# Performance work log

Hardware: AMD Instinct MI355X
Metric: run time of the kernel (lower is better)

## Reference

```python
import jax, jax.numpy as jnp
import numpy as np

E, D, H, T = 16, 1024, 4096, 8192  # num_expert, d_model, d_hidden (4h), total tokens


def setup_inputs() -> dict:
    key = jax.random.key(0)
    k0, k1, k2, k3, k4 = jax.random.split(key, 5)
    inp = jax.random.normal(k0, (T, D), dtype=jnp.float32)
    # FMoELinear init: kaiming-uniform-like, bound = 1/sqrt(fan_in)
    s1 = 1.0 / np.sqrt(D)
    s2 = 1.0 / np.sqrt(H)
    w1 = jax.random.uniform(k1, (E, H, D), jnp.float32, -s1, s1)  # htoh4 weight [E, out, in]
    b1 = jax.random.uniform(k2, (E, H), jnp.float32, -s1, s1)
    w2 = jax.random.uniform(k3, (E, D, H), jnp.float32, -s2, s2)  # h4toh weight
    b2 = jax.random.uniform(k4, (E, D), jnp.float32, -s2, s2)
    fwd_expert_count = jnp.full((E,), T // E, dtype=jnp.int32)  # tokens per expert (sums to T)
    return dict(inp=inp, w1=w1, b1=b1, w2=w2, b2=b2, fwd_expert_count=fwd_expert_count)


def reference(inp, w1, b1, w2, b2, fwd_expert_count):
    # Grouped GEMM: tokens are sorted by expert; segment e gets expert e's FFN.
    counts = np.asarray(fwd_expert_count)          # static per-expert row counts
    offs = np.concatenate([[0], np.cumsum(counts)])
    outs = []
    for e in range(counts.shape[0]):               # loop over fixed small expert set
        seg = inp[offs[e]:offs[e + 1]]             # [n_e, D]
        h = seg @ w1[e].T + b1[e]                  # htoh4: [n_e, H]
        h = jax.nn.gelu(h, approximate=False)      # torch F.gelu default (exact)
        outs.append(h @ w2[e].T + b2[e])           # h4toh: [n_e, D]
    return jnp.concatenate(outs, axis=0)           # [T, D]
```

## Files before the change

kernel.cpp:

```cpp
#include <hip/hip_runtime.h>
#include <hip/hip_bf16.h>

typedef float f32x4 __attribute__((ext_vector_type(4)));
typedef __bf16 bf16x8 __attribute__((ext_vector_type(8)));
typedef unsigned short u16;
typedef unsigned short u16x4 __attribute__((ext_vector_type(4)));
typedef unsigned short u16x8 __attribute__((ext_vector_type(8)));

#define BM 128
#define BN 128
#define BK 32
#define NT 256

__device__ __forceinline__ u16 f2bf(float f) {
  __bf16 h = (__bf16)f;
  return __builtin_bit_cast(u16, h);
}

template<bool A_BF16, bool DO_GELU, bool OUT_BF16>
__global__ __launch_bounds__(NT)
void ffn_gemm(const void* __restrict__ Ain, const float* __restrict__ Bw,
              const float* __restrict__ bias, void* __restrict__ Out,
              const int* __restrict__ counts, int E, int T, int N, int K)
{
  int mt = blockIdx.y;
  int row0 = 0, cnt = 0, e = 0;
  for (; e < E; ++e) {
    cnt = counts[e];
    int ntl = (cnt + BM - 1) / BM;
    if (mt < ntl) break;
    mt -= ntl; row0 += cnt;
  }
  if (e >= E) return;
  int valid = cnt - mt * BM; if (valid > BM) valid = BM;
  row0 += mt * BM;
  const int n0 = blockIdx.x * BN;

  const float* Be = Bw + (long long)e * N * K;
  const float* be = bias + (long long)e * N;

  __shared__ u16 As[2][BM][BK];
  __shared__ u16 Bs[2][BN][BK];

  const int t = threadIdx.x;
  const int lane = t & 63;
  const int w = t >> 6, wr = w >> 1, wc = w & 1;

  f32x4 acc[4][4];
#pragma unroll
  for (int i = 0; i < 4; ++i)
#pragma unroll
    for (int j = 0; j < 4; ++j) acc[i][j] = (f32x4){0.f, 0.f, 0.f, 0.f};

  const int NKT = K / BK;

  long long offA[4];
  if constexpr (!A_BF16) {
#pragma unroll
    for (int i = 0; i < 4; ++i) {
      int c = i * NT + t;
      int row = c >> 3, col = (c & 7) << 2;
      int gr = row0 + row; if (gr > T - 1) gr = T - 1;
      offA[i] = (long long)gr * K + col;
    }
  } else {
#pragma unroll
    for (int i = 0; i < 2; ++i) {
      int c = i * NT + t;
      int row = c >> 2, col = (c & 3) << 3;
      int gr = row0 + row; if (gr > T - 1) gr = T - 1;
      offA[i] = (long long)gr * K + col;
    }
  }
  long long offB[4];
#pragma unroll
  for (int i = 0; i < 4; ++i) {
    int c = i * NT + t;
    int row = c >> 3, col = (c & 7) << 2;
    offB[i] = (long long)(n0 + row) * K + col;
  }

  float rA[16]; u16x8 rAu[2]; float rB[16];

  auto load_g = [&](int kt) {
    const int k0 = kt * BK;
    if constexpr (!A_BF16) {
      const float* Af = (const float*)Ain;
#pragma unroll
      for (int i = 0; i < 4; ++i) {
        f32x4 v = *(const f32x4*)(Af + offA[i] + k0);
        rA[i*4+0] = v[0]; rA[i*4+1] = v[1]; rA[i*4+2] = v[2]; rA[i*4+3] = v[3];
      }
    } else {
      const u16* Ab = (const u16*)Ain;
#pragma unroll
      for (int i = 0; i < 2; ++i)
        rAu[i] = *(const u16x8*)(Ab + offA[i] + k0);
    }
#pragma unroll
    for (int i = 0; i < 4; ++i) {
      f32x4 v = *(const f32x4*)(Be + offB[i] + k0);
      rB[i*4+0] = v[0]; rB[i*4+1] = v[1]; rB[i*4+2] = v[2]; rB[i*4+3] = v[3];
    }
  };

  auto store_tile = [&](int buf) {
    if constexpr (!A_BF16) {
#pragma unroll
      for (int i = 0; i < 4; ++i) {
        int c = i * NT + t;
        int row = c >> 3, col = (c & 7) << 2;
        int kg = (col >> 3) ^ ((row >> 1) & 3);
        int off = kg * 8 + ((col >> 2) & 1) * 4;
        u16x4 pk = { f2bf(rA[i*4+0]), f2bf(rA[i*4+1]), f2bf(rA[i*4+2]), f2bf(rA[i*4+3]) };
        *(u16x4*)&As[buf][row][off] = pk;
      }
    } else {
#pragma unroll
      for (int i = 0; i < 2; ++i) {
        int c = i * NT + t;
        int row = c >> 2, col = (c & 3) << 3;
        int kg = (col >> 3) ^ ((row >> 1) & 3);
        *(u16x8*)&As[buf][row][kg * 8] = rAu[i];
      }
    }
#pragma unroll
    for (int i = 0; i < 4; ++i) {
      int c = i * NT + t;
      int row = c >> 3, col = (c & 7) << 2;
      int kg = (col >> 3) ^ ((row >> 1) & 3);
      int off = kg * 8 + ((col >> 2) & 1) * 4;
      u16x4 pk = { f2bf(rB[i*4+0]), f2bf(rB[i*4+1]), f2bf(rB[i*4+2]), f2bf(rB[i*4+3]) };
      *(u16x4*)&Bs[buf][row][off] = pk;
    }
  };

  load_g(0);
  store_tile(0);
  load_g(1);
  __syncthreads();

  for (int kt = 0; kt < NKT; ++kt) {
    const int cur = kt & 1;

    bf16x8 af[4], bfr[4];
    const int rl = lane & 15;
    const int kg = (lane >> 4) ^ ((rl >> 1) & 3);
#pragma unroll
    for (int mf = 0; mf < 4; ++mf)
      af[mf] = __builtin_bit_cast(bf16x8, *(const u16x8*)&As[cur][wr*64 + mf*16 + rl][kg*8]);
#pragma unroll
    for (int nf = 0; nf < 4; ++nf)
      bfr[nf] = __builtin_bit_cast(bf16x8, *(const u16x8*)&Bs[cur][wc*64 + nf*16 + rl][kg*8]);

    if (kt + 1 < NKT) store_tile(cur ^ 1);
    if (kt + 2 < NKT) load_g(kt + 2);

#pragma unroll
    for (int mf = 0; mf < 4; ++mf)
#pragma unroll
      for (int nf = 0; nf < 4; ++nf)
        acc[mf][nf] = __builtin_amdgcn_mfma_f32_16x16x32_bf16(af[mf], bfr[nf], acc[mf][nf], 0, 0, 0);

    if (kt + 1 < NKT) __syncthreads();
  }

  const int cl = lane & 15, rg = lane >> 4;
#pragma unroll
  for (int mf = 0; mf < 4; ++mf) {
#pragma unroll
    for (int nf = 0; nf < 4; ++nf) {
      int gcol = n0 + wc*64 + nf*16 + cl;
      float bv = be[gcol];
#pragma unroll
      for (int r = 0; r < 4; ++r) {
        int lrow = wr*64 + mf*16 + rg*4 + r;
        if (lrow < valid) {
          float v = acc[mf][nf][r] + bv;
          if constexpr (DO_GELU)
            v = 0.5f * v * (1.0f + erff(v * 0.70710678118654752f));
          long long idx = (long long)(row0 + lrow) * N + gcol;
          if constexpr (OUT_BF16) ((u16*)Out)[idx] = f2bf(v);
          else                    ((float*)Out)[idx] = v;
        }
      }
    }
  }
}

extern "C" void kernel_launch(void* const* d_in, const int* in_sizes, int n_in,
                              void* d_out, int out_size, void* d_ws, size_t ws_size,
                              hipStream_t stream) {
  const float* inp = (const float*)d_in[0];
  const float* w1  = (const float*)d_in[1];
  const float* b1  = (const float*)d_in[2];
  const float* w2  = (const float*)d_in[3];
  const float* b2  = (const float*)d_in[4];
  const int* cnts  = (const int*)d_in[5];

  const int E = in_sizes[5];
  const int H = in_sizes[2] / E;
  const int D = in_sizes[4] / E;
  const int T = in_sizes[0] / D;

  u16* hbuf = (u16*)d_ws;

  const int tiles = (T + BM - 1) / BM + E;
  dim3 blk(NT);

  dim3 g1(H / BN, tiles);
  ffn_gemm<false, true, true><<<g1, blk, 0, stream>>>(
      (const void*)inp, w1, b1, (void*)hbuf, cnts, E, T, H, D);

  dim3 g2(D / BN, tiles);
  ffn_gemm<true, false, false><<<g2, blk, 0, stream>>>(
      (const void*)hbuf, w2, b2, d_out, cnts, E, T, D, H);
}
```

Before: 328.8 us.

## Add dedicated 256x256-tile kernel for first FFN GEMM with 8 waves

Adds a specialized kernel for the first GEMM (input times w1, with GELU) that uses 256x256 output tiles, 512 threads and 8x4 MFMA fragments per wave. Each wave now reads from LDS a larger share of the operands it computes with, and the fp32 global traffic per FLOP drops, since the fp32 loads and bf16 conversion happen in the mainloop. It also precomputes swizzled LDS offsets and raises wave priority around the MFMA block. The cost is a much larger accumulator register footprint (128 floats per thread), which may lower occupancy. There are also fewer blocks (16 column tiles by 48 row tiles), which could underfill the GPU.

```diff
diff --git a/kernel.cpp b/kernel.cpp
--- a/kernel.cpp
+++ b/kernel.cpp
@@ -7,15 +7,156 @@
 typedef unsigned short u16x4 __attribute__((ext_vector_type(4)));
 typedef unsigned short u16x8 __attribute__((ext_vector_type(8)));
 
+__device__ __forceinline__ u16 f2bf(float f) {
+  __bf16 h = (__bf16)f;
+  return __builtin_bit_cast(u16, h);
+}
+
+#define G1_BM 256
+#define G1_BN 256
+#define G1_BK 32
+#define G1_NT 512
+
+__global__ __launch_bounds__(G1_NT, 2)
+void ffn_gemm1(const float* __restrict__ Af, const float* __restrict__ Bw,
+               const float* __restrict__ bias, u16* __restrict__ Out,
+               const int* __restrict__ counts, int E, int T, int N, int K)
+{
+  int mt = blockIdx.y;
+  int row0 = 0, cnt = 0, e = 0;
+  for (; e < E; ++e) {
+    cnt = counts[e];
+    int ntl = (cnt + G1_BM - 1) / G1_BM;
+    if (mt < ntl) break;
+    mt -= ntl; row0 += cnt;
+  }
+  if (e >= E) return;
+  int valid = cnt - mt * G1_BM; if (valid > G1_BM) valid = G1_BM;
+  row0 += mt * G1_BM;
+  const int n0 = blockIdx.x * G1_BN;
+  const float* Be = Bw + (long long)e * N * K;
+  const float* be = bias + (long long)e * N;
+
+  __shared__ u16 As[2][G1_BM * G1_BK];
+  __shared__ u16 Bs[2][G1_BN * G1_BK];
+
+  const int t = threadIdx.x;
+  const int lane = t & 63;
+  const int w = t >> 6, wr = w >> 2, wc = w & 3;
+
+  f32x4 acc[8][4];
+#pragma unroll
+  for (int i = 0; i < 8; ++i)
+#pragma unroll
+    for (int j = 0; j < 4; ++j) acc[i][j] = (f32x4){0.f, 0.f, 0.f, 0.f};
+
+  const int NKT = K / G1_BK;
+
+  long long offA[4]; int wAo[4];
+  long long offB[4]; int wBo[4];
+#pragma unroll
+  for (int i = 0; i < 4; ++i) {
+    int idx = i * G1_NT + t;
+    int row = idx >> 3, col4 = idx & 7;
+    int gr = row0 + row; if (gr > T - 1) gr = T - 1;
+    offA[i] = (long long)gr * K + col4 * 4;
+    wAo[i] = row * G1_BK + (((col4 >> 1) ^ (row & 3)) << 3) + ((col4 & 1) << 2);
+    offB[i] = (long long)(n0 + row) * K + col4 * 4;
+    wBo[i] = wAo[i] - ((row0 + row <= T - 1 ? 0 : 0));
+    wBo[i] = row * G1_BK + (((col4 >> 1) ^ (row & 3)) << 3) + ((col4 & 1) << 2);
+  }
+
+  const int rl = lane & 15, kgr = lane >> 4;
+  int aoff[8], boff[4];
+#pragma unroll
+  for (int mf = 0; mf < 8; ++mf) {
+    int row = wr * 128 + mf * 16 + rl;
+    aoff[mf] = row * G1_BK + ((kgr ^ (rl & 3)) << 3);
+  }
+#pragma unroll
+  for (int nf = 0; nf < 4; ++nf) {
+    int row = wc * 64 + nf * 16 + rl;
+    boff[nf] = row * G1_BK + ((kgr ^ (rl & 3)) << 3);
+  }
+
+  f32x4 a4[4], b4[4];
+
+  auto load_g = [&](int kt) {
+    const int k0 = kt * G1_BK;
+#pragma unroll
+    for (int i = 0; i < 4; ++i) a4[i] = *(const f32x4*)(Af + offA[i] + k0);
+#pragma unroll
+    for (int i = 0; i < 4; ++i) b4[i] = *(const f32x4*)(Be + offB[i] + k0);
+  };
+
+  auto store_tile = [&](int buf) {
+#pragma unroll
+    for (int i = 0; i < 4; ++i) {
+      u16x4 pa = { f2bf(a4[i][0]), f2bf(a4[i][1]), f2bf(a4[i][2]), f2bf(a4[i][3]) };
+      *(u16x4*)&As[buf][wAo[i]] = pa;
+    }
+#pragma unroll
+    for (int i = 0; i < 4; ++i) {
+      u16x4 pb = { f2bf(b4[i][0]), f2bf(b4[i][1]), f2bf(b4[i][2]), f2bf(b4[i][3]) };
+      *(u16x4*)&Bs[buf][wBo[i]] = pb;
+    }
+  };
+
+  load_g(0);
+  store_tile(0);
+  load_g(1);
+  __syncthreads();
+
+#pragma unroll 2
+  for (int kt = 0; kt < NKT; ++kt) {
+    const int cur = kt & 1;
+
+    bf16x8 bfr[4], af[8];
+#pragma unroll
+    for (int nf = 0; nf < 4; ++nf)
+      bfr[nf] = __builtin_bit_cast(bf16x8, *(const u16x8*)&Bs[cur][boff[nf]]);
+#pragma unroll
+    for (int mf = 0; mf < 8; ++mf)
+      af[mf] = __builtin_bit_cast(bf16x8, *(const u16x8*)&As[cur][aoff[mf]]);
+
+    if (kt + 1 < NKT) store_tile(cur ^ 1);
+    if (kt + 2 < NKT) load_g(kt + 2);
+
+    __builtin_amdgcn_s_setprio(1);
+#pragma unroll
+    for (int mf = 0; mf < 8; ++mf)
+#pragma unroll
+      for (int nf = 0; nf < 4; ++nf)
+        acc[mf][nf] = __builtin_amdgcn_mfma_f32_16x16x32_bf16(af[mf], bfr[nf], acc[mf][nf], 0, 0, 0);
+    __builtin_amdgcn_s_setprio(0);
+
+    __syncthreads();
+  }
+
+  const int cl = lane & 15, rg = lane >> 4;
+#pragma unroll
+  for (int nf = 0; nf < 4; ++nf) {
+    int gcol = n0 + wc * 64 + nf * 16 + cl;
+    float bv = be[gcol];
+#pragma unroll
+    for (int mf = 0; mf < 8; ++mf) {
+#pragma unroll
+      for (int r = 0; r < 4; ++r) {
+        int lrow = wr * 128 + mf * 16 + rg * 4 + r;
+        if (lrow < valid) {
+          float v = acc[mf][nf][r] + bv;
+          v = 0.5f * v * (1.0f + erff(v * 0.70710678118654752f));
+          Out[(long long)(row0 + lrow) * N + gcol] = f2bf(v);
+        }
+      }
+    }
+  }
+}
+
 #define BM 128
 #define BN 128
 #define BK 32
 #define NT 256
-
-__device__ __forceinline__ u16 f2bf(float f) {
-  __bf16 h = (__bf16)f;
-  return __builtin_bit_cast(u16, h);
-}
 
 template<bool A_BF16, bool DO_GELU, bool OUT_BF16>
 __global__ __launch_bounds__(NT)
@@ -205,14 +346,12 @@
 
   u16* hbuf = (u16*)d_ws;
 
-  const int tiles = (T + BM - 1) / BM + E;
-  dim3 blk(NT);
-
-  dim3 g1(H / BN, tiles);
-  ffn_gemm<false, true, true><<<g1, blk, 0, stream>>>(
-      (const void*)inp, w1, b1, (void*)hbuf, cnts, E, T, H, D);
-
-  dim3 g2(D / BN, tiles);
-  ffn_gemm<true, false, false><<<g2, blk, 0, stream>>>(
+  const int tiles1 = (T + G1_BM - 1) / G1_BM + E;
+  dim3 g1(H / G1_BN, tiles1);
+  ffn_gemm1<<<g1, dim3(G1_NT), 0, stream>>>(inp, w1, b1, hbuf, cnts, E, T, H, D);
+
+  const int tiles2 = (T + BM - 1) / BM + E;
+  dim3 g2(D / BN, tiles2);
+  ffn_gemm<true, false, false><<<g2, dim3(NT), 0, stream>>>(
       (const void*)hbuf, w2, b2, d_out, cnts, E, T, D, H);
 }
```

Result: faster. 315.3 us (-4.1%).

## Pre-convert input to bf16 and loop multiple N tiles per block in GEMM1

Applied to the files above, without the earlier changes.

Adds a separate kernel that converts the fp32 input activations to bf16 once, so the first GEMM reads bf16 A tiles instead of converting fp32 in every block. The first GEMM now has each block process four consecutive N tiles, shrinking the grid and reusing the block's expert lookup. The expert lookup loads the counts into a register array with vector loads. Costs are an extra launch and more workspace, and a smaller grid for GEMM1 that may reduce occupancy, with the same B weight traffic.

```diff
diff --git a/kernel.cpp b/kernel.cpp
--- a/kernel.cpp
+++ b/kernel.cpp
@@ -2,6 +2,7 @@
 #include <hip/hip_bf16.h>
 
 typedef float f32x4 __attribute__((ext_vector_type(4)));
+typedef int   i32x4 __attribute__((ext_vector_type(4)));
 typedef __bf16 bf16x8 __attribute__((ext_vector_type(8)));
 typedef unsigned short u16;
 typedef unsigned short u16x4 __attribute__((ext_vector_type(4)));
@@ -11,30 +12,53 @@
 #define BN 128
 #define BK 32
 #define NT 256
+#define MAXE 32
 
 __device__ __forceinline__ u16 f2bf(float f) {
   __bf16 h = (__bf16)f;
   return __builtin_bit_cast(u16, h);
 }
 
-template<bool A_BF16, bool DO_GELU, bool OUT_BF16>
+__global__ __launch_bounds__(256)
+void cvt_bf16(const float* __restrict__ in, u16* __restrict__ out, int n8) {
+  int i = blockIdx.x * 256 + threadIdx.x;
+  if (i < n8) {
+    f32x4 a = *(const f32x4*)(in + (long long)i * 8);
+    f32x4 b = *(const f32x4*)(in + (long long)i * 8 + 4);
+    u16x8 r = { f2bf(a[0]), f2bf(a[1]), f2bf(a[2]), f2bf(a[3]),
+                f2bf(b[0]), f2bf(b[1]), f2bf(b[2]), f2bf(b[3]) };
+    *(u16x8*)(out + (long long)i * 8) = r;
+  }
+}
+
+template<bool DO_GELU, bool OUT_BF16, int NTB>
 __global__ __launch_bounds__(NT)
-void ffn_gemm(const void* __restrict__ Ain, const float* __restrict__ Bw,
+void ffn_gemm(const u16* __restrict__ Ain, const float* __restrict__ Bw,
               const float* __restrict__ bias, void* __restrict__ Out,
               const int* __restrict__ counts, int E, int T, int N, int K)
 {
-  int mt = blockIdx.y;
-  int row0 = 0, cnt = 0, e = 0;
-  for (; e < E; ++e) {
-    cnt = counts[e];
-    int ntl = (cnt + BM - 1) / BM;
-    if (mt < ntl) break;
-    mt -= ntl; row0 += cnt;
-  }
-  if (e >= E) return;
+  int cs[MAXE];
+#pragma unroll
+  for (int j = 0; j < MAXE / 4; ++j) {
+    if (j * 4 + 3 < E) {
+      *(i32x4*)&cs[j * 4] = *(const i32x4*)(counts + j * 4);
+    } else {
+#pragma unroll
+      for (int q = 0; q < 4; ++q) cs[j*4+q] = (j*4+q < E) ? counts[j*4+q] : 0;
+    }
+  }
+  int mt = blockIdx.y, row0 = 0, e = -1, cnt = 0;
+#pragma unroll
+  for (int i = 0; i < MAXE; ++i) {
+    if (i < E && e < 0) {
+      int ntl = (cs[i] + BM - 1) / BM;
+      if (mt < ntl) { e = i; cnt = cs[i]; }
+      else { mt -= ntl; row0 += cs[i]; }
+    }
+  }
+  if (e < 0) return;
   int valid = cnt - mt * BM; if (valid > BM) valid = BM;
   row0 += mt * BM;
-  const int n0 = blockIdx.x * BN;
 
   const float* Be = Bw + (long long)e * N * K;
   const float* be = bias + (long long)e * N;
@@ -45,143 +69,121 @@
   const int t = threadIdx.x;
   const int lane = t & 63;
   const int w = t >> 6, wr = w >> 1, wc = w & 1;
-
-  f32x4 acc[4][4];
-#pragma unroll
-  for (int i = 0; i < 4; ++i)
-#pragma unroll
-    for (int j = 0; j < 4; ++j) acc[i][j] = (f32x4){0.f, 0.f, 0.f, 0.f};
-
   const int NKT = K / BK;
 
-  long long offA[4];
-  if constexpr (!A_BF16) {
-#pragma unroll
-    for (int i = 0; i < 4; ++i) {
-      int c = i * NT + t;
-      int row = c >> 3, col = (c & 7) << 2;
-      int gr = row0 + row; if (gr > T - 1) gr = T - 1;
-      offA[i] = (long long)gr * K + col;
-    }
-  } else {
-#pragma unroll
-    for (int i = 0; i < 2; ++i) {
-      int c = i * NT + t;
-      int row = c >> 2, col = (c & 3) << 3;
-      int gr = row0 + row; if (gr > T - 1) gr = T - 1;
-      offA[i] = (long long)gr * K + col;
-    }
-  }
-  long long offB[4];
+  long long offA[2];
+#pragma unroll
+  for (int i = 0; i < 2; ++i) {
+    int c = i * NT + t;
+    int row = c >> 2, col = (c & 3) << 3;
+    int gr = row0 + row; if (gr > T - 1) gr = T - 1;
+    offA[i] = (long long)gr * K + col;
+  }
+  int rBrow[4], rBcol[4];
 #pragma unroll
   for (int i = 0; i < 4; ++i) {
     int c = i * NT + t;
-    int row = c >> 3, col = (c & 7) << 2;
-    offB[i] = (long long)(n0 + row) * K + col;
-  }
-
-  float rA[16]; u16x8 rAu[2]; float rB[16];
-
-  auto load_g = [&](int kt) {
-    const int k0 = kt * BK;
-    if constexpr (!A_BF16) {
-      const float* Af = (const float*)Ain;
+    rBrow[i] = c >> 3; rBcol[i] = (c & 7) << 2;
+  }
+
+  const int rl = lane & 15;
+  const int kgf = (lane >> 4) ^ ((rl >> 1) & 3);
+  const int cl = lane & 15, rg = lane >> 4;
+
+  u16x8 rAu[2]; float rB[16];
+
+  for (int pass = 0; pass < NTB; ++pass) {
+    const int n0 = (blockIdx.x * NTB + pass) * BN;
+
+    long long offB[4];
+#pragma unroll
+    for (int i = 0; i < 4; ++i)
+      offB[i] = (long long)(n0 + rBrow[i]) * K + rBcol[i];
+
+    f32x4 acc[4][4];
+#pragma unroll
+    for (int i = 0; i < 4; ++i)
+#pragma unroll
+      for (int j = 0; j < 4; ++j) acc[i][j] = (f32x4){0.f, 0.f, 0.f, 0.f};
+
+    auto load_g = [&](int kt) {
+      const int k0 = kt * BK;
+#pragma unroll
+      for (int i = 0; i < 2; ++i)
+        rAu[i] = *(const u16x8*)(Ain + offA[i] + k0);
 #pragma unroll
       for (int i = 0; i < 4; ++i) {
-        f32x4 v = *(const f32x4*)(Af + offA[i] + k0);
-        rA[i*4+0] = v[0]; rA[i*4+1] = v[1]; rA[i*4+2] = v[2]; rA[i*4+3] = v[3];
-      }
-    } else {
-      const u16* Ab = (const u16*)Ain;
-#pragma unroll
-      for (int i = 0; i < 2; ++i)
-        rAu[i] = *(const u16x8*)(Ab + offA[i] + k0);
-    }
-#pragma unroll
-    for (int i = 0; i < 4; ++i) {
-      f32x4 v = *(const f32x4*)(Be + offB[i] + k0);
-      rB[i*4+0] = v[0]; rB[i*4+1] = v[1]; rB[i*4+2] = v[2]; rB[i*4+3] = v[3];
-    }
-  };
-
-  auto store_tile = [&](int buf) {
-    if constexpr (!A_BF16) {
+        f32x4 v = *(const f32x4*)(Be + offB[i] + k0);
+        rB[i*4+0] = v[0]; rB[i*4+1] = v[1]; rB[i*4+2] = v[2]; rB[i*4+3] = v[3];
+      }
+    };
+
+    auto store_tile = [&](int buf) {
+#pragma unroll
+      for (int i = 0; i < 2; ++i) {
+        int c = i * NT + t;
+        int row = c >> 2, col = (c & 3) << 3;
+        int kg = (col >> 3) ^ ((row >> 1) & 3);
+        *(u16x8*)&As[buf][row][kg * 8] = rAu[i];
+      }
 #pragma unroll
       for (int i = 0; i < 4; ++i) {
         int c = i * NT + t;
         int row = c >> 3, col = (c & 7) << 2;
         int kg = (col >> 3) ^ ((row >> 1) & 3);
         int off = kg * 8 + ((col >> 2) & 1) * 4;
-        u16x4 pk = { f2bf(rA[i*4+0]), f2bf(rA[i*4+1]), f2bf(rA[i*4+2]), f2bf(rA[i*4+3]) };
-        *(u16x4*)&As[buf][row][off] = pk;
-      }
-    } else {
-#pragma unroll
-      for (int i = 0; i < 2; ++i) {
-        int c = i * NT + t;
-        int row = c >> 2, col = (c & 3) << 3;
-        int kg = (col >> 3) ^ ((row >> 1) & 3);
-        *(u16x8*)&As[buf][row][kg * 8] = rAu[i];
-      }
-    }
-#pragma unroll
-    for (int i = 0; i < 4; ++i) {
-      int c = i * NT + t;
-      int row = c >> 3, col = (c & 7) << 2;
-      int kg = (col >> 3) ^ ((row >> 1) & 3);
-      int off = kg * 8 + ((col >> 2) & 1) * 4;
-      u16x4 pk = { f2bf(rB[i*4+0]), f2bf(rB[i*4+1]), f2bf(rB[i*4+2]), f2bf(rB[i*4+3]) };
-      *(u16x4*)&Bs[buf][row][off] = pk;
-    }
-  };
-
-  load_g(0);
-  store_tile(0);
-  load_g(1);
-  __syncthreads();
-
-  for (int kt = 0; kt < NKT; ++kt) {
-    const int cur = kt & 1;
-
-    bf16x8 af[4], bfr[4];
-    const int rl = lane & 15;
-    const int kg = (lane >> 4) ^ ((rl >> 1) & 3);
-#pragma unroll
-    for (int mf = 0; mf < 4; ++mf)
-      af[mf] = __builtin_bit_cast(bf16x8, *(const u16x8*)&As[cur][wr*64 + mf*16 + rl][kg*8]);
-#pragma unroll
-    for (int nf = 0; nf < 4; ++nf)
-      bfr[nf] = __builtin_bit_cast(bf16x8, *(const u16x8*)&Bs[cur][wc*64 + nf*16 + rl][kg*8]);
-
-    if (kt + 1 < NKT) store_tile(cur ^ 1);
-    if (kt + 2 < NKT) load_g(kt + 2);
-
-#pragma unroll
-    for (int mf = 0; mf < 4; ++mf)
+        u16x4 pk = { f2bf(rB[i*4+0]), f2bf(rB[i*4+1]), f2bf(rB[i*4+2]), f2bf(rB[i*4+3]) };
+        *(u16x4*)&Bs[buf][row][off] = pk;
+      }
+    };
+
+    if (NTB > 1 && pass > 0) __syncthreads();
+
+    load_g(0);
+    store_tile(0);
+    load_g(1);
+    __syncthreads();
+
+    for (int kt = 0; kt < NKT; ++kt) {
+      const int cur = kt & 1;
+
+      bf16x8 af[4], bfr[4];
+#pragma unroll
+      for (int mf = 0; mf < 4; ++mf)
+        af[mf] = __builtin_bit_cast(bf16x8, *(const u16x8*)&As[cur][wr*64 + mf*16 + rl][kgf*8]);
 #pragma unroll
       for (int nf = 0; nf < 4; ++nf)
-        acc[mf][nf] = __builtin_amdgcn_mfma_f32_16x16x32_bf16(af[mf], bfr[nf], acc[mf][nf], 0, 0, 0);
-
-    if (kt + 1 < NKT) __syncthreads();
-  }
-
-  const int cl = lane & 15, rg = lane >> 4;
-#pragma unroll
-  for (int mf = 0; mf < 4; ++mf) {
-#pragma unroll
-    for (int nf = 0; nf < 4; ++nf) {
-      int gcol = n0 + wc*64 + nf*16 + cl;
-      float bv = be[gcol];
-#pragma unroll
-      for (int r = 0; r < 4; ++r) {
-        int lrow = wr*64 + mf*16 + rg*4 + r;
-        if (lrow < valid) {
-          float v = acc[mf][nf][r] + bv;
-          if constexpr (DO_GELU)
-            v = 0.5f * v * (1.0f + erff(v * 0.70710678118654752f));
-          long long idx = (long long)(row0 + lrow) * N + gcol;
-          if constexpr (OUT_BF16) ((u16*)Out)[idx] = f2bf(v);
-          else                    ((float*)Out)[idx] = v;
+        bfr[nf] = __builtin_bit_cast(bf16x8, *(const u16x8*)&Bs[cur][wc*64 + nf*16 + rl][kgf*8]);
+
+      if (kt + 1 < NKT) store_tile(cur ^ 1);
+      if (kt + 2 < NKT) load_g(kt + 2);
+
+#pragma unroll
+      for (int mf = 0; mf < 4; ++mf)
+#pragma unroll
+        for (int nf = 0; nf < 4; ++nf)
+          acc[mf][nf] = __builtin_amdgcn_mfma_f32_16x16x32_bf16(af[mf], bfr[nf], acc[mf][nf], 0, 0, 0);
+
+      if (kt + 1 < NKT) __syncthreads();
+    }
+
+#pragma unroll
+    for (int mf = 0; mf < 4; ++mf) {
+#pragma unroll
+      for (int nf = 0; nf < 4; ++nf) {
+        int gcol = n0 + wc*64 + nf*16 + cl;
+        float bv = be[gcol];
+#pragma unroll
+        for (int r = 0; r < 4; ++r) {
+          int lrow = wr*64 + mf*16 + rg*4 + r;
+          if (lrow < valid) {
+            float v = acc[mf][nf][r] + bv;
+            if constexpr (DO_GELU)
+              v = 0.5f * v * (1.0f + erff(v * 0.70710678118654752f));
+            long long idx = (long long)(row0 + lrow) * N + gcol;
+            if constexpr (OUT_BF16) ((u16*)Out)[idx] = f2bf(v);
+            else                    ((float*)Out)[idx] = v;
+          }
         }
       }
     }
@@ -204,15 +206,19 @@
   const int T = in_sizes[0] / D;
 
   u16* hbuf = (u16*)d_ws;
+  u16* ibuf = (u16*)((char*)d_ws + (size_t)T * H * 2);
+
+  const int n8 = (T * D) / 8;
+  cvt_bf16<<<dim3((n8 + 255) / 256), dim3(256), 0, stream>>>(inp, ibuf, n8);
 
   const int tiles = (T + BM - 1) / BM + E;
-  dim3 blk(NT);
-
-  dim3 g1(H / BN, tiles);
-  ffn_gemm<false, true, true><<<g1, blk, 0, stream>>>(
-      (const void*)inp, w1, b1, (void*)hbuf, cnts, E, T, H, D);
+
+  constexpr int NTB1 = 4;
+  dim3 g1(H / BN / NTB1, tiles);
+  ffn_gemm<true, true, NTB1><<<g1, dim3(NT), 0, stream>>>(
+      ibuf, w1, b1, (void*)hbuf, cnts, E, T, H, D);
 
   dim3 g2(D / BN, tiles);
-  ffn_gemm<true, false, false><<<g2, blk, 0, stream>>>(
-      (const void*)hbuf, w2, b2, d_out, cnts, E, T, D, H);
-}
+  ffn_gemm<false, false, 1><<<g2, dim3(NT), 0, stream>>>(
+      hbuf, w2, b2, d_out, cnts, E, T, D, H);
+}
```

New measurement: 351.9 us. +7.0%, slower.
